# Performance work log

Measured on AMD Instinct MI355X. Metric: run time of the kernel, lower is better.

Reference implementation:

```python
import jax, jax.numpy as jnp
import numpy as np


def _sparsify24(w):
    """2:4 structured sparsity: per contiguous group of 4 along the last dim,
    keep the 2 largest-magnitude entries, zero the other 2 (soft_threshold24)."""
    m, n = w.shape
    g = w.reshape(m, n // 4, 4)
    a = jnp.abs(g)
    # 2nd-largest magnitude in each group = index 2 of ascending sort of 4
    thresh = jnp.sort(a, axis=-1)[..., 2:3]
    mask = a >= thresh
    return (g * mask).reshape(m, n)


def setup_inputs() -> dict:
    key = jax.random.key(0)
    k1, k2, k3 = jax.random.split(key, 3)
    B, S, DIN, DOUT = 4, 4096, 1024, 1024
    x = jax.random.normal(k1, (B, S, DIN), dtype=jnp.float32)
    weight = jax.random.normal(k2, (DIN, DOUT), dtype=jnp.float32) * 0.02
    bias = jax.random.normal(k3, (DOUT,), dtype=jnp.float32) * 0.02
    sparse_scale = jnp.ones((1,), dtype=jnp.float32)
    return {"x": x, "weight": weight, "bias": bias, "sparse_scale": sparse_scale}


def reference(x, weight, bias, sparse_scale):
    # get_sparse_weight: cast weight to fp16, apply 2:4 sparsity, multiply by
    # learnable fp32 scale (promotes to fp32 as in torch half*float).
    w_sparse = _sparsify24(weight.astype(jnp.float16)).astype(jnp.float32) * sparse_scale
    # fake_fp8_mm: both operands cast to fp16, accumulate/output in fp32.
    a = x.reshape(-1, x.shape[-1]).astype(jnp.float16)          # [B*S, DIN]
    b = w_sparse.astype(jnp.float16)                             # [DIN, DOUT]
    out = jnp.matmul(a, b, preferred_element_type=jnp.float32)   # [B*S, DOUT] fp32
    out = out.reshape(*x.shape[:-1], -1) + bias
    return out
```

## Files before the change

### kernel.cpp

```cpp
#include <hip/hip_runtime.h>
#include <hip/hip_fp16.h>
#include <stdint.h>

#define M_TOT 16384
#define N_TOT 1024
#define K_TOT 1024

typedef _Float16 f16x8 __attribute__((ext_vector_type(8)));
typedef float f32x4 __attribute__((ext_vector_type(4)));

__device__ inline void gl2lds16(const void* g, void* l) {
    __builtin_amdgcn_global_load_lds(
        (const __attribute__((address_space(1))) void*)(uintptr_t)(g),
        (__attribute__((address_space(3))) void*)(uint32_t)(uintptr_t)(l),
        16, 0, 0);
}

__global__ void prep_weight(const float* __restrict__ W,
                            const float* __restrict__ scale_p,
                            _Float16* __restrict__ wT) {
    const float scale = scale_p[0];
    int idx = blockIdx.x * blockDim.x + threadIdx.x;
    int k = idx & (K_TOT - 1);
    int g = idx >> 10;
    float4 w4 = *(const float4*)&W[(size_t)k * N_TOT + g * 4];
    _Float16 h0 = (_Float16)w4.x, h1 = (_Float16)w4.y, h2 = (_Float16)w4.z, h3 = (_Float16)w4.w;
    float a0 = fabsf((float)h0), a1 = fabsf((float)h1), a2 = fabsf((float)h2), a3 = fabsf((float)h3);
    float lo01 = fminf(a0, a1), hi01 = fmaxf(a0, a1);
    float lo23 = fminf(a2, a3), hi23 = fmaxf(a2, a3);
    float s2 = fmaxf(fminf(hi01, hi23), fmaxf(lo01, lo23));
    float v0 = (a0 >= s2) ? (float)h0 : 0.0f;
    float v1 = (a1 >= s2) ? (float)h1 : 0.0f;
    float v2 = (a2 >= s2) ? (float)h2 : 0.0f;
    float v3 = (a3 >= s2) ? (float)h3 : 0.0f;
    size_t nb = (size_t)(g * 4) * K_TOT + k;
    wT[nb + 0 * K_TOT] = (_Float16)(v0 * scale);
    wT[nb + 1 * K_TOT] = (_Float16)(v1 * scale);
    wT[nb + 2 * K_TOT] = (_Float16)(v2 * scale);
    wT[nb + 3 * K_TOT] = (_Float16)(v3 * scale);
}

__global__ void cast_x(const float* __restrict__ X, _Float16* __restrict__ Xh) {
    size_t i = ((size_t)blockIdx.x * blockDim.x + threadIdx.x) * 8;
    float4 x0 = *(const float4*)&X[i];
    float4 x1 = *(const float4*)&X[i + 4];
    f16x8 h;
    h[0] = (_Float16)x0.x; h[1] = (_Float16)x0.y; h[2] = (_Float16)x0.z; h[3] = (_Float16)x0.w;
    h[4] = (_Float16)x1.x; h[5] = (_Float16)x1.y; h[6] = (_Float16)x1.z; h[7] = (_Float16)x1.w;
    *(f16x8*)&Xh[i] = h;
}

__global__ void __launch_bounds__(256) gemm_bt(const _Float16* __restrict__ A,
                                               const _Float16* __restrict__ Bt,
                                               const float* __restrict__ bias,
                                               float* __restrict__ C) {
    __shared__ _Float16 sA[128 * 32];
    __shared__ _Float16 sB[128 * 32];
    const int tid = threadIdx.x;
    const int id = blockIdx.x;
    const int by = id & 127;
    const int bx = id >> 7;
    const int wave = tid >> 6;
    const int lane = tid & 63;
    const int wm = wave >> 1, wn = wave & 1;
    const int quad = lane >> 4;
    const int l16 = lane & 15;

    const int srow = tid >> 2;
    const int scol = (tid & 3) * 8;

    const _Float16* gA = A + ((size_t)(by * 128 + srow)) * K_TOT + scol;
    const _Float16* gB = Bt + ((size_t)(bx * 128 + srow)) * K_TOT + scol;
    _Float16* lA = sA + srow * 32 + scol;
    _Float16* lB = sB + srow * 32 + scol;

    f32x4 acc[4][4];
#pragma unroll
    for (int i = 0; i < 4; ++i)
#pragma unroll
        for (int j = 0; j < 4; ++j)
            acc[i][j] = (f32x4){0.f, 0.f, 0.f, 0.f};

    for (int k0 = 0; k0 < K_TOT; k0 += 32) {
        __syncthreads();
        gl2lds16(gA + k0, lA);
        gl2lds16(gA + k0 + (size_t)64 * K_TOT, lA + 64 * 32);
        gl2lds16(gB + k0, lB);
        gl2lds16(gB + k0 + (size_t)64 * K_TOT, lB + 64 * 32);
        __syncthreads();

        f16x8 af[4], bf[4];
#pragma unroll
        for (int i = 0; i < 4; ++i) {
            af[i] = *(const f16x8*)&sA[(wm * 64 + i * 16 + l16) * 32 + quad * 8];
            bf[i] = *(const f16x8*)&sB[(wn * 64 + i * 16 + l16) * 32 + quad * 8];
        }
#pragma unroll
        for (int i = 0; i < 4; ++i)
#pragma unroll
            for (int j = 0; j < 4; ++j)
                acc[i][j] = __builtin_amdgcn_mfma_f32_16x16x32_f16(af[i], bf[j], acc[i][j], 0, 0, 0);
    }

#pragma unroll
    for (int j = 0; j < 4; ++j) {
        const int col = bx * 128 + wn * 64 + j * 16 + l16;
        const float bj = bias[col];
#pragma unroll
        for (int i = 0; i < 4; ++i) {
            const int row0 = by * 128 + wm * 64 + i * 16 + quad * 4;
#pragma unroll
            for (int r = 0; r < 4; ++r) {
                __builtin_nontemporal_store(acc[i][j][r] + bj,
                                            &C[(size_t)(row0 + r) * N_TOT + col]);
            }
        }
    }
}

extern "C" void kernel_launch(void* const* d_in, const int* in_sizes, int n_in,
                              void* d_out, int out_size, void* d_ws, size_t ws_size,
                              hipStream_t stream) {
    const float* x      = (const float*)d_in[0];
    const float* weight = (const float*)d_in[1];
    const float* bias   = (const float*)d_in[2];
    const float* sscale = (const float*)d_in[3];
    float* out = (float*)d_out;

    _Float16* wT = (_Float16*)d_ws;
    _Float16* xh = (_Float16*)((char*)d_ws + (size_t)2 * 1024 * 1024);

    prep_weight<<<(K_TOT * N_TOT / 4) / 256, 256, 0, stream>>>(weight, sscale, wT);
    cast_x<<<(M_TOT * K_TOT / 8) / 256, 256, 0, stream>>>(x, xh);
    gemm_bt<<<1024, 256, 0, stream>>>(xh, wT, bias, out);
}
```

Baseline: 179.4 us.

## Fuse fp32-to-fp16 cast of x into GEMM with double-buffered LDS

Removes the separate cast kernel and has the GEMM load fp32 activations directly, converting to fp16 in registers before storing to shared memory. Shared tiles are double-buffered so next-tile loads overlap MFMA work, with one barrier per iteration. This avoids writing and re-reading an fp16 copy of x, at the cost of reading fp32 A tiles (twice the bytes) repeatedly across column blocks. Output stores switch from nontemporal to regular stores.

```diff
diff --git a/kernel.cpp b/kernel.cpp
--- a/kernel.cpp
+++ b/kernel.cpp
@@ -40,22 +40,12 @@
     wT[nb + 3 * K_TOT] = (_Float16)(v3 * scale);
 }
 
-__global__ void cast_x(const float* __restrict__ X, _Float16* __restrict__ Xh) {
-    size_t i = ((size_t)blockIdx.x * blockDim.x + threadIdx.x) * 8;
-    float4 x0 = *(const float4*)&X[i];
-    float4 x1 = *(const float4*)&X[i + 4];
-    f16x8 h;
-    h[0] = (_Float16)x0.x; h[1] = (_Float16)x0.y; h[2] = (_Float16)x0.z; h[3] = (_Float16)x0.w;
-    h[4] = (_Float16)x1.x; h[5] = (_Float16)x1.y; h[6] = (_Float16)x1.z; h[7] = (_Float16)x1.w;
-    *(f16x8*)&Xh[i] = h;
-}
-
-__global__ void __launch_bounds__(256) gemm_bt(const _Float16* __restrict__ A,
-                                               const _Float16* __restrict__ Bt,
-                                               const float* __restrict__ bias,
-                                               float* __restrict__ C) {
-    __shared__ _Float16 sA[128 * 32];
-    __shared__ _Float16 sB[128 * 32];
+__global__ void __launch_bounds__(256) gemm_fused(const float* __restrict__ X,
+                                                  const _Float16* __restrict__ Bt,
+                                                  const float* __restrict__ bias,
+                                                  float* __restrict__ C) {
+    __shared__ _Float16 sA[2][128 * 32];
+    __shared__ _Float16 sB[2][128 * 32];
     const int tid = threadIdx.x;
     const int id = blockIdx.x;
     const int by = id & 127;
@@ -66,13 +56,15 @@
     const int quad = lane >> 4;
     const int l16 = lane & 15;
 
+    const int arow = tid >> 1;
+    const int acol = (tid & 1) * 16;
+    const float* gA = X + ((size_t)(by * 128 + arow)) * K_TOT + acol;
+    const int aoff = arow * 32 + acol;
+
     const int srow = tid >> 2;
     const int scol = (tid & 3) * 8;
-
-    const _Float16* gA = A + ((size_t)(by * 128 + srow)) * K_TOT + scol;
     const _Float16* gB = Bt + ((size_t)(bx * 128 + srow)) * K_TOT + scol;
-    _Float16* lA = sA + srow * 32 + scol;
-    _Float16* lB = sB + srow * 32 + scol;
+    const int boff = srow * 32 + scol;
 
     f32x4 acc[4][4];
 #pragma unroll
@@ -81,25 +73,55 @@
         for (int j = 0; j < 4; ++j)
             acc[i][j] = (f32x4){0.f, 0.f, 0.f, 0.f};
 
+    {
+        float4 a0 = *(const float4*)(gA + 0);
+        float4 a1 = *(const float4*)(gA + 4);
+        float4 a2 = *(const float4*)(gA + 8);
+        float4 a3 = *(const float4*)(gA + 12);
+        gl2lds16(gB, &sB[0][boff]);
+        gl2lds16(gB + (size_t)64 * K_TOT, &sB[0][boff + 64 * 32]);
+        f16x8 h0, h1;
+        h0[0] = (_Float16)a0.x; h0[1] = (_Float16)a0.y; h0[2] = (_Float16)a0.z; h0[3] = (_Float16)a0.w;
+        h0[4] = (_Float16)a1.x; h0[5] = (_Float16)a1.y; h0[6] = (_Float16)a1.z; h0[7] = (_Float16)a1.w;
+        h1[0] = (_Float16)a2.x; h1[1] = (_Float16)a2.y; h1[2] = (_Float16)a2.z; h1[3] = (_Float16)a2.w;
+        h1[4] = (_Float16)a3.x; h1[5] = (_Float16)a3.y; h1[6] = (_Float16)a3.z; h1[7] = (_Float16)a3.w;
+        *(f16x8*)&sA[0][aoff] = h0;
+        *(f16x8*)&sA[0][aoff + 8] = h1;
+    }
+
+#pragma unroll 2
     for (int k0 = 0; k0 < K_TOT; k0 += 32) {
+        const int cur = (k0 >> 5) & 1;
+        const int nxt = cur ^ 1;
         __syncthreads();
-        gl2lds16(gA + k0, lA);
-        gl2lds16(gA + k0 + (size_t)64 * K_TOT, lA + 64 * 32);
-        gl2lds16(gB + k0, lB);
-        gl2lds16(gB + k0 + (size_t)64 * K_TOT, lB + 64 * 32);
-        __syncthreads();
+
+        const int kn = (k0 + 32 < K_TOT) ? (k0 + 32) : 0;
+        float4 a0 = *(const float4*)(gA + kn);
+        float4 a1 = *(const float4*)(gA + kn + 4);
+        float4 a2 = *(const float4*)(gA + kn + 8);
+        float4 a3 = *(const float4*)(gA + kn + 12);
+        gl2lds16(gB + kn, &sB[nxt][boff]);
+        gl2lds16(gB + kn + (size_t)64 * K_TOT, &sB[nxt][boff + 64 * 32]);
 
         f16x8 af[4], bf[4];
 #pragma unroll
         for (int i = 0; i < 4; ++i) {
-            af[i] = *(const f16x8*)&sA[(wm * 64 + i * 16 + l16) * 32 + quad * 8];
-            bf[i] = *(const f16x8*)&sB[(wn * 64 + i * 16 + l16) * 32 + quad * 8];
+            af[i] = *(const f16x8*)&sA[cur][(wm * 64 + i * 16 + l16) * 32 + quad * 8];
+            bf[i] = *(const f16x8*)&sB[cur][(wn * 64 + i * 16 + l16) * 32 + quad * 8];
         }
 #pragma unroll
         for (int i = 0; i < 4; ++i)
 #pragma unroll
             for (int j = 0; j < 4; ++j)
                 acc[i][j] = __builtin_amdgcn_mfma_f32_16x16x32_f16(af[i], bf[j], acc[i][j], 0, 0, 0);
+
+        f16x8 h0, h1;
+        h0[0] = (_Float16)a0.x; h0[1] = (_Float16)a0.y; h0[2] = (_Float16)a0.z; h0[3] = (_Float16)a0.w;
+        h0[4] = (_Float16)a1.x; h0[5] = (_Float16)a1.y; h0[6] = (_Float16)a1.z; h0[7] = (_Float16)a1.w;
+        h1[0] = (_Float16)a2.x; h1[1] = (_Float16)a2.y; h1[2] = (_Float16)a2.z; h1[3] = (_Float16)a2.w;
+        h1[4] = (_Float16)a3.x; h1[5] = (_Float16)a3.y; h1[6] = (_Float16)a3.z; h1[7] = (_Float16)a3.w;
+        *(f16x8*)&sA[nxt][aoff] = h0;
+        *(f16x8*)&sA[nxt][aoff + 8] = h1;
     }
 
 #pragma unroll
@@ -111,8 +133,7 @@
             const int row0 = by * 128 + wm * 64 + i * 16 + quad * 4;
 #pragma unroll
             for (int r = 0; r < 4; ++r) {
-                __builtin_nontemporal_store(acc[i][j][r] + bj,
-                                            &C[(size_t)(row0 + r) * N_TOT + col]);
+                C[(size_t)(row0 + r) * N_TOT + col] = acc[i][j][r] + bj;
             }
         }
     }
@@ -128,9 +149,7 @@
     float* out = (float*)d_out;
 
     _Float16* wT = (_Float16*)d_ws;
-    _Float16* xh = (_Float16*)((char*)d_ws + (size_t)2 * 1024 * 1024);
 
     prep_weight<<<(K_TOT * N_TOT / 4) / 256, 256, 0, stream>>>(weight, sscale, wT);
-    cast_x<<<(M_TOT * K_TOT / 8) / 256, 256, 0, stream>>>(x, xh);
-    gemm_bt<<<1024, 256, 0, stream>>>(xh, wT, bias, out);
+    gemm_fused<<<1024, 256, 0, stream>>>(x, wT, bias, out);
 }
```

After: 183.5 us. 1.02x slower.
